# Kernel tuning notes

Hardware: AMD Instinct MI355X
Metric: run time of the kernel (lower is better)

## Reference

```python
import jax, jax.numpy as jnp
from jax import lax
import numpy as np

T, B, D, H = 4096, 32, 512, 256


def setup_inputs() -> dict:
    key = jax.random.key(0)
    ks = jax.random.split(key, 8)
    s_ih = 1.0 / np.sqrt(H)
    inp = {
        "x": jax.random.normal(ks[0], (T, B, D), dtype=jnp.float32),
        "reset": jax.random.randint(ks[1], (T, B), 0, 2, dtype=jnp.int32),
        # PyTorch nn.LSTM params, gate order (i, f, g, o)
        "W_ih": jax.random.uniform(ks[2], (4 * H, D), jnp.float32, -s_ih, s_ih),
        "W_hh": jax.random.uniform(ks[3], (4 * H, H), jnp.float32, -s_ih, s_ih),
        "b_ih": jax.random.uniform(ks[4], (4 * H,), jnp.float32, -s_ih, s_ih),
        "b_hh": jax.random.uniform(ks[5], (4 * H,), jnp.float32, -s_ih, s_ih),
        "W_proj": jax.random.uniform(ks[6], (1, H), jnp.float32, -s_ih, s_ih),
        "b_proj": jax.random.uniform(ks[7], (1,), jnp.float32, -s_ih, s_ih),
    }
    return inp


def _lstm_with_reset(x, reset, W_ih, W_hh, b_ih, b_hh):
    # Precompute input contribution for all timesteps: [T, B, 4H]
    xW = jnp.einsum("tbd,gd->tbg", x, W_ih) + b_ih + b_hh
    h0 = jnp.zeros((x.shape[1], H), x.dtype)
    c0 = jnp.zeros((x.shape[1], H), x.dtype)

    def step(carry, inp):
        h, c = carry
        xw, r = inp
        keep = (1 - r).astype(h.dtype)[:, None]  # zero state at episode starts
        h = h * keep
        c = c * keep
        gates = xw + h @ W_hh.T  # [B, 4H]
        i, f, g, o = jnp.split(gates, 4, axis=-1)
        c = jax.nn.sigmoid(f) * c + jax.nn.sigmoid(i) * jnp.tanh(g)
        h = jax.nn.sigmoid(o) * jnp.tanh(c)
        return (h, c), h

    (_, _), hs = lax.scan(step, (h0, c0), (xW, reset))
    return hs  # [T, B, H]


def reference(x, reset, W_ih, W_hh, b_ih, b_hh, W_proj, b_proj):
    hs = _lstm_with_reset(x, reset, W_ih, W_hh, b_ih, b_hh)
    return hs @ W_proj.T + b_proj  # [T, B, 1]
```

## Files before the change

### kernel.cpp

```cpp
#include <hip/hip_runtime.h>
#include <cstdint>
#include <cstddef>

#define T_DIM 4096
#define B_DIM 32
#define D_DIM 512
#define H_DIM 256
#define G_DIM 1024
#define HSTR 264

typedef _Float16 h8 __attribute__((ext_vector_type(8)));
typedef float f4 __attribute__((ext_vector_type(4)));

__global__ void seg_build_kernel(const int* __restrict__ reset,
                                 unsigned* __restrict__ starts,
                                 unsigned* __restrict__ segcnt) {
  __shared__ unsigned cnts[256];
  __shared__ unsigned offs[256];
  const int b = blockIdx.x;
  const int tid = threadIdx.x;
  const int t0 = tid * 16;
  unsigned c = 0;
  for (int e = 0; e < 16; ++e) {
    int t = t0 + e;
    bool pred = (t == 0) || (reset[t * B_DIM + b] != 0);
    c += pred ? 1u : 0u;
  }
  cnts[tid] = c;
  __syncthreads();
  if (tid == 0) {
    unsigned run = 0;
    for (int i = 0; i < 256; ++i) { unsigned v = cnts[i]; offs[i] = run; run += v; }
    segcnt[b] = run;
  }
  __syncthreads();
  unsigned o = (unsigned)b * 4096u + offs[tid];
  for (int e = 0; e < 16; ++e) {
    int t = t0 + e;
    bool pred = (t == 0) || (reset[t * B_DIM + b] != 0);
    if (pred) { starts[o++] = (unsigned)t; }
  }
}

__global__ void seg_flat_kernel(const unsigned* __restrict__ starts,
                                const unsigned* __restrict__ segcnt,
                                uint2* __restrict__ flat,
                                unsigned* __restrict__ meta) {
  __shared__ unsigned offs;
  const int b = blockIdx.x;
  const int tid = threadIdx.x;
  if (tid == 0) {
    unsigned o = 0;
    for (int i = 0; i < b; ++i) o += segcnt[i];
    offs = o;
    if (b == 31) meta[1] = o + segcnt[31];
    if (b == 0) meta[0] = 0u;
  }
  __syncthreads();
  const unsigned cnt = segcnt[b];
  const unsigned off = offs;
  for (unsigned s = tid; s < cnt; s += 256) {
    unsigned t0 = starts[b * 4096u + s];
    unsigned t1 = (s + 1 < cnt) ? starts[b * 4096u + s + 1] : 4096u;
    flat[off + s] = make_uint2(t0 | ((unsigned)b << 16), t1);
  }
}

__global__ void wpack_kernel(const float* __restrict__ Whh,
                             _Float16* __restrict__ wpack) {
  int gid = blockIdx.x * 256 + threadIdx.x;
  int nt = gid >> 9;
  int rem = gid & 511;
  int ks = rem >> 6;
  int l = rem & 63;
  int n = nt * 16 + (l & 15);
  int k = ks * 32 + (l >> 4) * 8;
  const float* src = Whh + (size_t)n * H_DIM + k;
  f4 v0 = *(const f4*)src;
  f4 v1 = *(const f4*)(src + 4);
  h8 wv = {(_Float16)v0.x, (_Float16)v0.y, (_Float16)v0.z, (_Float16)v0.w,
           (_Float16)v1.x, (_Float16)v1.y, (_Float16)v1.z, (_Float16)v1.w};
  *(h8*)(wpack + (size_t)gid * 8) = wv;
}

#define BM 128
#define BN 128
#define BK 32

__global__ __launch_bounds__(256) void xw_gemm_kernel(
    const float* __restrict__ X, const float* __restrict__ Wih,
    const float* __restrict__ bih, const float* __restrict__ bhh,
    _Float16* __restrict__ xw) {
  __shared__ _Float16 As[BM * BK];
  __shared__ _Float16 Bs[BN * BK];
  const int tid = threadIdx.x;
  const int lane = tid & 63;
  const int wave = tid >> 6;
  const size_t m0 = (size_t)blockIdx.y * BM;
  const int n0 = blockIdx.x * BN;
  const int wm = (wave & 1) * 64;
  const int wn = (wave >> 1) * 64;
  const int q = lane >> 4;
  const int r = lane & 15;

  f4 acc[4][4];
#pragma unroll
  for (int i = 0; i < 4; ++i)
#pragma unroll
    for (int j = 0; j < 4; ++j) { f4 z = {0.f, 0.f, 0.f, 0.f}; acc[i][j] = z; }

  const int srow = tid >> 1;
  const int kh = (tid & 1) * 16;

  for (int k0 = 0; k0 < D_DIM; k0 += BK) {
    const float* ax = X + (m0 + (size_t)srow) * D_DIM + k0 + kh;
    const float* bx = Wih + ((size_t)(n0 + srow)) * D_DIM + k0 + kh;
    f4 a0 = *(const f4*)(ax);
    f4 a1 = *(const f4*)(ax + 4);
    f4 a2 = *(const f4*)(ax + 8);
    f4 a3 = *(const f4*)(ax + 12);
    f4 b0 = *(const f4*)(bx);
    f4 b1 = *(const f4*)(bx + 4);
    f4 b2 = *(const f4*)(bx + 8);
    f4 b3 = *(const f4*)(bx + 12);
    h8 ha0 = {(_Float16)a0.x, (_Float16)a0.y, (_Float16)a0.z, (_Float16)a0.w,
              (_Float16)a1.x, (_Float16)a1.y, (_Float16)a1.z, (_Float16)a1.w};
    h8 ha1 = {(_Float16)a2.x, (_Float16)a2.y, (_Float16)a2.z, (_Float16)a2.w,
              (_Float16)a3.x, (_Float16)a3.y, (_Float16)a3.z, (_Float16)a3.w};
    h8 hb0 = {(_Float16)b0.x, (_Float16)b0.y, (_Float16)b0.z, (_Float16)b0.w,
              (_Float16)b1.x, (_Float16)b1.y, (_Float16)b1.z, (_Float16)b1.w};
    h8 hb1 = {(_Float16)b2.x, (_Float16)b2.y, (_Float16)b2.z, (_Float16)b2.w,
              (_Float16)b3.x, (_Float16)b3.y, (_Float16)b3.z, (_Float16)b3.w};
    *(h8*)(As + srow * BK + kh) = ha0;
    *(h8*)(As + srow * BK + kh + 8) = ha1;
    *(h8*)(Bs + srow * BK + kh) = hb0;
    *(h8*)(Bs + srow * BK + kh + 8) = hb1;
    __syncthreads();

    h8 af[4], bf[4];
#pragma unroll
    for (int mi = 0; mi < 4; ++mi)
      af[mi] = *(const h8*)(As + (wm + mi * 16 + r) * BK + q * 8);
#pragma unroll
    for (int ni = 0; ni < 4; ++ni)
      bf[ni] = *(const h8*)(Bs + (wn + ni * 16 + r) * BK + q * 8);
#pragma unroll
    for (int mi = 0; mi < 4; ++mi)
#pragma unroll
      for (int ni = 0; ni < 4; ++ni)
        acc[mi][ni] = __builtin_amdgcn_mfma_f32_16x16x32_f16(af[mi], bf[ni], acc[mi][ni], 0, 0, 0);
    __syncthreads();
  }

#pragma unroll
  for (int mi = 0; mi < 4; ++mi) {
#pragma unroll
    for (int ni = 0; ni < 4; ++ni) {
      int n = n0 + wn + ni * 16 + r;
      float bias = bih[n] + bhh[n];
#pragma unroll
      for (int reg = 0; reg < 4; ++reg) {
        size_t m = m0 + (size_t)(wm + mi * 16 + q * 4 + reg);
        xw[m * G_DIM + n] = (_Float16)(acc[mi][ni][reg] + bias);
      }
    }
  }
}

__device__ __forceinline__ float sigmf(float x) { return 1.f / (1.f + __expf(-x)); }
__device__ __forceinline__ float tanhf_(float x) {
  float e = __expf(-2.f * fabsf(x));
  float r = (1.f - e) / (1.f + e);
  return copysignf(r, x);
}
__device__ __forceinline__ f4 MF(h8 a, h8 b, f4 c) {
  return __builtin_amdgcn_mfma_f32_16x16x32_f16(a, b, c, 0, 0, 0);
}

#define WPK(g, ks) ((const h8*)(wpack + (((size_t)(((g)*16 + w) * 8 + (ks))) * 64 + l) * 8))
#define WLD(g, ks2) (*(const h8*)(Wlds + ((((ks2)*64) + ((g)*16 + w)) * 64 + l) * 8))
#define ARD(mt, ks) (*(const h8*)(Hbuf + (16*(mt) + r16) * HSTR + (ks)*32 + q*8))

#define MFMA8(B0, B1, B2, B3, KS)                          \
  a0 = ARD(0, KS); a1 = ARD(1, KS);                        \
  acc00 = MF(a0, B0, acc00); acc10 = MF(a1, B0, acc10);    \
  acc01 = MF(a0, B1, acc01); acc11 = MF(a1, B1, acc11);    \
  acc02 = MF(a0, B2, acc02); acc12 = MF(a1, B2, acc12);    \
  acc03 = MF(a0, B3, acc03); acc13 = MF(a1, B3, acc13);

#define XWADD(ACC, RB, G) {                                          \
  int nb = (G)*512 + nbase2;                                         \
  f4 xv;                                                             \
  xv.x = (float)*(const _Float16*)(xwc + RB.x + nb);                 \
  xv.y = (float)*(const _Float16*)(xwc + RB.y + nb);                 \
  xv.z = (float)*(const _Float16*)(xwc + RB.z + nb);                 \
  xv.w = (float)*(const _Float16*)(xwc + RB.w + nb);                 \
  ACC += xv; }

#define CONTROL_STEP do {                                                    \
  int m = tid;                                                               \
  if (alivef[m]) {                                                           \
    unsigned oi = outix[m];                                                  \
    if (oi != 0xFFFFFFFFu) {                                                 \
      float s = bp;                                                          \
      _Pragma("unroll") for (int ww = 0; ww < 16; ++ww) s += pbuf[ww][m];    \
      out[oi] = s;                                                           \
    }                                                                        \
    int t = tcur[m] + 1;                                                     \
    if (t < tend[m]) {                                                       \
      tcur[m] = t; keepm[m] = 1.f;                                           \
      unsigned row = (unsigned)t * 32u + (unsigned)bcol[m];                  \
      trowB[m] = row * 2048u; outix[m] = row;                                \
    } else {                                                                 \
      unsigned idx = atomicAdd(ctr, 1u);                                     \
      if (idx < nseg) {                                                      \
        uint2 sg = flat[idx];                                                \
        int t0s = (int)(sg.x & 0xFFFFu); int bb = (int)(sg.x >> 16);         \
        tcur[m] = t0s; tend[m] = (int)sg.y; bcol[m] = bb; keepm[m] = 0.f;    \
        unsigned row = (unsigned)t0s * 32u + (unsigned)bb;                   \
        trowB[m] = row * 2048u; outix[m] = row;                              \
        h8 zz = {0,0,0,0,0,0,0,0};                                           \
        _Pragma("unroll") for (int i2 = 0; i2 < 33; ++i2)                    \
          *(h8*)(Hbuf + (size_t)m * HSTR + i2 * 8) = zz;                     \
      } else {                                                               \
        alivef[m] = 0; outix[m] = 0xFFFFFFFFu; trowB[m] = 0;                 \
        keepm[m] = 0.f;                                                      \
      }                                                                      \
    }                                                                        \
  }                                                                          \
} while (0)

__global__ __launch_bounds__(1024, 4) void lstm_scan_mfma(
    const _Float16* __restrict__ xw,
    const _Float16* __restrict__ wpack,
    const float* __restrict__ Wproj,
    const float* __restrict__ bproj,
    const uint2* __restrict__ flat,
    unsigned* __restrict__ meta,
    float* __restrict__ out) {
  __shared__ __align__(16) _Float16 Wlds[2 * 64 * 64 * 8];
  __shared__ __align__(16) _Float16 Hbuf[32 * HSTR];
  __shared__ __align__(16) float pbuf[16][32];
  __shared__ __align__(16) unsigned trowB[32];
  __shared__ __align__(16) float keepm[32];
  __shared__ unsigned outix[32];
  __shared__ int tcur[32], tend[32], bcol[32], alivef[32];

  const int tid = threadIdx.x;
  const int l = tid & 63;
  const int w = tid >> 6;
  const int q = l >> 4;
  const int r16 = l & 15;
  const int hh = 16 * w + r16;
  const int nbase2 = hh * 2;
  const char* xwc = (const char*)xw;
  unsigned* ctr = meta;
  const unsigned nseg = meta[1];

  for (int it = 0; it < 8; ++it) {
    int idx = it * 1024 + tid;
    int ks2 = idx >> 12;
    int nt = (idx >> 6) & 63;
    int ll = idx & 63;
    *(h8*)(Wlds + (size_t)idx * 8) =
        *(const h8*)(wpack + (((size_t)(nt * 8 + ks2 + 1)) * 64 + ll) * 8);
  }
  for (int i = tid; i < 32 * HSTR / 8; i += 1024) {
    h8 z = {0,0,0,0,0,0,0,0};
    *(h8*)(Hbuf + (size_t)i * 8) = z;
  }
  h8 wb0 = *WPK(0, 0), wb1 = *WPK(1, 0), wb2 = *WPK(2, 0), wb3 = *WPK(3, 0);
  const float wpv = Wproj[hh];
  const float bp = bproj[0];
  if (tid < 32) {
    alivef[tid] = 1; tcur[tid] = 0; tend[tid] = 0; bcol[tid] = 0;
    outix[tid] = 0xFFFFFFFFu; trowB[tid] = 0; keepm[tid] = 0.f;
  }
  float cst[8] = {0, 0, 0, 0, 0, 0, 0, 0};
  float pr[8];
  __syncthreads();
  if (tid < 32) CONTROL_STEP;
  int nalive = __syncthreads_count(tid < 32 ? alivef[tid] : 0);

  while (nalive > 0) {
    f4 z4 = {0.f, 0.f, 0.f, 0.f};
    f4 acc00 = z4, acc01 = z4, acc02 = z4, acc03 = z4;
    f4 acc10 = z4, acc11 = z4, acc12 = z4, acc13 = z4;
    h8 a0, a1;
    h8 s0 = *WPK(0, 3), s1 = *WPK(1, 3), s2 = *WPK(2, 3), s3 = *WPK(3, 3);
    MFMA8(wb0, wb1, wb2, wb3, 0)
    h8 u0 = *WPK(0, 4), u1 = *WPK(1, 4), u2 = *WPK(2, 4), u3 = *WPK(3, 4);
    { h8 b0 = WLD(0, 0), b1 = WLD(1, 0), b2 = WLD(2, 0), b3 = WLD(3, 0);
      MFMA8(b0, b1, b2, b3, 1) }
    { h8 b0 = WLD(0, 1), b1 = WLD(1, 1), b2 = WLD(2, 1), b3 = WLD(3, 1);
      MFMA8(b0, b1, b2, b3, 2) }
    MFMA8(s0, s1, s2, s3, 3)
    s0 = *WPK(0, 5); s1 = *WPK(1, 5); s2 = *WPK(2, 5); s3 = *WPK(3, 5);
    MFMA8(u0, u1, u2, u3, 4)
    u0 = *WPK(0, 6); u1 = *WPK(1, 6); u2 = *WPK(2, 6); u3 = *WPK(3, 6);
    MFMA8(s0, s1, s2, s3, 5)
    s0 = *WPK(0, 7); s1 = *WPK(1, 7); s2 = *WPK(2, 7); s3 = *WPK(3, 7);
    MFMA8(u0, u1, u2, u3, 6)
    MFMA8(s0, s1, s2, s3, 7)

    __syncthreads();

    uint4 rb0 = *(const uint4*)&trowB[q * 4];
    uint4 rb1 = *(const uint4*)&trowB[16 + q * 4];
    XWADD(acc00, rb0, 0) XWADD(acc01, rb0, 1) XWADD(acc02, rb0, 2) XWADD(acc03, rb0, 3)
    XWADD(acc10, rb1, 0) XWADD(acc11, rb1, 1) XWADD(acc12, rb1, 2) XWADD(acc13, rb1, 3)

    f4 kp0 = *(const f4*)&keepm[q * 4];
    f4 kp1 = *(const f4*)&keepm[16 + q * 4];
#pragma unroll
    for (int r = 0; r < 4; ++r) {
      float gi = sigmf(acc00[r]);
      float gf = sigmf(acc01[r]);
      float gg = tanhf_(acc02[r]);
      float go = sigmf(acc03[r]);
      float cn = gf * (cst[r] * kp0[r]) + gi * gg;
      cst[r] = cn;
      float hv = go * tanhf_(cn);
      Hbuf[(q * 4 + r) * HSTR + hh] = (_Float16)hv;
      pr[r] = hv * wpv;
    }
#pragma unroll
    for (int r = 0; r < 4; ++r) {
      float gi = sigmf(acc10[r]);
      float gf = sigmf(acc11[r]);
      float gg = tanhf_(acc12[r]);
      float go = sigmf(acc13[r]);
      float cn = gf * (cst[4 + r] * kp1[r]) + gi * gg;
      cst[4 + r] = cn;
      float hv = go * tanhf_(cn);
      Hbuf[(16 + q * 4 + r) * HSTR + hh] = (_Float16)hv;
      pr[4 + r] = hv * wpv;
    }
#pragma unroll
    for (int j = 0; j < 8; ++j) {
      pr[j] += __shfl_xor(pr[j], 1);
      pr[j] += __shfl_xor(pr[j], 2);
      pr[j] += __shfl_xor(pr[j], 4);
      pr[j] += __shfl_xor(pr[j], 8);
    }
    if (r16 == 0) {
#pragma unroll
      for (int j = 0; j < 8; ++j)
        pbuf[w][16 * (j >> 2) + q * 4 + (j & 3)] = pr[j];
    }

    __syncthreads();
    if (tid < 32) CONTROL_STEP;
    nalive = __syncthreads_count(tid < 32 ? alivef[tid] : 0);
  }
}

extern "C" void kernel_launch(void* const* d_in, const int* in_sizes, int n_in,
                              void* d_out, int out_size, void* d_ws, size_t ws_size,
                              hipStream_t stream) {
  const float* x = (const float*)d_in[0];
  const int* reset = (const int*)d_in[1];
  const float* Wih = (const float*)d_in[2];
  const float* Whh = (const float*)d_in[3];
  const float* bih = (const float*)d_in[4];
  const float* bhh = (const float*)d_in[5];
  const float* Wproj = (const float*)d_in[6];
  const float* bproj = (const float*)d_in[7];
  float* out = (float*)d_out;

  char* ws = (char*)d_ws;
  _Float16* xw = (_Float16*)ws;
  unsigned* starts = (unsigned*)(ws + 268435456ULL);
  unsigned* segcnt = (unsigned*)(ws + 268959744ULL);
  uint2* flat = (uint2*)(ws + 268959872ULL);
  _Float16* wpack = (_Float16*)(ws + 270008448ULL);
  unsigned* meta = (unsigned*)(ws + 270532736ULL);

  hipLaunchKernelGGL(seg_build_kernel, dim3(32), dim3(256), 0, stream,
                     reset, starts, segcnt);
  hipLaunchKernelGGL(seg_flat_kernel, dim3(32), dim3(256), 0, stream,
                     starts, segcnt, flat, meta);
  hipLaunchKernelGGL(wpack_kernel, dim3(128), dim3(256), 0, stream,
                     Whh, wpack);
  hipLaunchKernelGGL(xw_gemm_kernel, dim3(8, 1024), dim3(256), 0, stream,
                     x, Wih, bih, bhh, xw);
  hipLaunchKernelGGL(lstm_scan_mfma, dim3(256), dim3(1024), 0, stream,
                     xw, wpack, Wproj, bproj, flat, meta, out);
}
```

Measured before the change: 1.446 ms.

## Sort segments by length, halve scan block size, remap GEMM tiles per XCD

Adds a counting sort that orders reset-delimited segments longest-first, so the dynamic work queue in the scan kernel schedules long segments early and trims tail imbalance. The scan kernel drops from 1024 to 512 threads; each wave now handles twice as many hidden columns and keeps 4 of the 8 K-slices of W_hh in registers. The remaining slices are split between two streamed from global memory and two held in LDS. The xW GEMM grid is flattened and remapped so neighbouring tiles land on the same XCD for better L2 reuse, and sigmoid/tanh switch to a fast reciprocal form. These changes raise register pressure and add a serial single-block sort kernel, and the new tanh form may lose accuracy for large inputs.

```diff
diff --git a/kernel.cpp b/kernel.cpp
--- a/kernel.cpp
+++ b/kernel.cpp
@@ -8,17 +8,20 @@
 #define H_DIM 256
 #define G_DIM 1024
 #define HSTR 264
+#define NBUCK 128
 
 typedef _Float16 h8 __attribute__((ext_vector_type(8)));
 typedef float f4 __attribute__((ext_vector_type(4)));
 
 __global__ void seg_build_kernel(const int* __restrict__ reset,
                                  unsigned* __restrict__ starts,
-                                 unsigned* __restrict__ segcnt) {
+                                 unsigned* __restrict__ segcnt,
+                                 unsigned* __restrict__ hist) {
   __shared__ unsigned cnts[256];
   __shared__ unsigned offs[256];
   const int b = blockIdx.x;
   const int tid = threadIdx.x;
+  if (b == 0 && tid < NBUCK) hist[tid] = 0u;
   const int t0 = tid * 16;
   unsigned c = 0;
   for (int e = 0; e < 16; ++e) {
@@ -44,7 +47,8 @@
 
 __global__ void seg_flat_kernel(const unsigned* __restrict__ starts,
                                 const unsigned* __restrict__ segcnt,
-                                uint2* __restrict__ flat,
+                                uint2* __restrict__ flat2,
+                                unsigned* __restrict__ hist,
                                 unsigned* __restrict__ meta) {
   __shared__ unsigned offs;
   const int b = blockIdx.x;
@@ -62,7 +66,30 @@
   for (unsigned s = tid; s < cnt; s += 256) {
     unsigned t0 = starts[b * 4096u + s];
     unsigned t1 = (s + 1 < cnt) ? starts[b * 4096u + s + 1] : 4096u;
-    flat[off + s] = make_uint2(t0 | ((unsigned)b << 16), t1);
+    flat2[off + s] = make_uint2(t0 | ((unsigned)b << 16), t1);
+    unsigned len = t1 - t0;
+    atomicAdd(&hist[min(len, (unsigned)NBUCK) - 1u], 1u);
+  }
+}
+
+__global__ void seg_sort_kernel(const uint2* __restrict__ flat2,
+                                const unsigned* __restrict__ hist,
+                                uint2* __restrict__ flat,
+                                const unsigned* __restrict__ meta) {
+  __shared__ unsigned cur[NBUCK];
+  const unsigned nseg = meta[1];
+  const int tid = threadIdx.x;
+  if (tid == 0) {
+    unsigned run = 0;
+    for (int k = NBUCK - 1; k >= 0; --k) { cur[k] = run; run += hist[k]; }
+  }
+  __syncthreads();
+  for (unsigned i = tid; i < nseg; i += 1024) {
+    uint2 e = flat2[i];
+    unsigned len = e.y - (e.x & 0xFFFFu);
+    unsigned bk = min(len, (unsigned)NBUCK) - 1u;
+    unsigned pos = atomicAdd(&cur[bk], 1u);
+    flat[pos] = e;
   }
 }
 
@@ -96,8 +123,11 @@
   const int tid = threadIdx.x;
   const int lane = tid & 63;
   const int wave = tid >> 6;
-  const size_t m0 = (size_t)blockIdx.y * BM;
-  const int n0 = blockIdx.x * BN;
+  const unsigned wg = blockIdx.x;
+  const unsigned xcd = wg & 7u;
+  const unsigned idx = wg >> 3;
+  const size_t m0 = (size_t)(xcd * 128u + (idx >> 3)) * BM;
+  const int n0 = (int)(idx & 7u) * BN;
   const int wm = (wave & 1) * 64;
   const int wn = (wave >> 1) * 64;
   const int q = lane >> 4;
@@ -167,35 +197,60 @@
   }
 }
 
-__device__ __forceinline__ float sigmf(float x) { return 1.f / (1.f + __expf(-x)); }
+__device__ __forceinline__ float sigmf(float x) {
+  return __builtin_amdgcn_rcpf(1.f + __expf(-x));
+}
 __device__ __forceinline__ float tanhf_(float x) {
-  float e = __expf(-2.f * fabsf(x));
-  float r = (1.f - e) / (1.f + e);
-  return copysignf(r, x);
+  return 2.f * __builtin_amdgcn_rcpf(1.f + __expf(-2.f * x)) - 1.f;
 }
 __device__ __forceinline__ f4 MF(h8 a, h8 b, f4 c) {
   return __builtin_amdgcn_mfma_f32_16x16x32_f16(a, b, c, 0, 0, 0);
 }
 
-#define WPK(g, ks) ((const h8*)(wpack + (((size_t)(((g)*16 + w) * 8 + (ks))) * 64 + l) * 8))
-#define WLD(g, ks2) (*(const h8*)(Wlds + ((((ks2)*64) + ((g)*16 + w)) * 64 + l) * 8))
+#define WPKp(g, j, ks) \
+  ((const h8*)(wpack + (((size_t)((((g)*16 + 2*w + (j)) * 8 + (ks))) * 64 + l) * 8)))
+#define WLDp(g, j, ks2) \
+  (*(const h8*)(Wlds + ((((ks2)*64) + ((g)*16 + 2*w + (j))) * 64 + l) * 8))
 #define ARD(mt, ks) (*(const h8*)(Hbuf + (16*(mt) + r16) * HSTR + (ks)*32 + q*8))
 
-#define MFMA8(B0, B1, B2, B3, KS)                          \
-  a0 = ARD(0, KS); a1 = ARD(1, KS);                        \
-  acc00 = MF(a0, B0, acc00); acc10 = MF(a1, B0, acc10);    \
-  acc01 = MF(a0, B1, acc01); acc11 = MF(a1, B1, acc11);    \
-  acc02 = MF(a0, B2, acc02); acc12 = MF(a1, B2, acc12);    \
-  acc03 = MF(a0, B3, acc03); acc13 = MF(a1, B3, acc13);
-
-#define XWADD(ACC, RB, G) {                                          \
-  int nb = (G)*512 + nbase2;                                         \
-  f4 xv;                                                             \
-  xv.x = (float)*(const _Float16*)(xwc + RB.x + nb);                 \
-  xv.y = (float)*(const _Float16*)(xwc + RB.y + nb);                 \
-  xv.z = (float)*(const _Float16*)(xwc + RB.z + nb);                 \
-  xv.w = (float)*(const _Float16*)(xwc + RB.w + nb);                 \
-  ACC += xv; }
+#define MFK_REG(KS) do {                                                   \
+  h8 a0_ = ARD(0, KS), a1_ = ARD(1, KS);                                   \
+  _Pragma("unroll") for (int g = 0; g < 4; ++g)                            \
+  _Pragma("unroll") for (int j = 0; j < 2; ++j) {                          \
+    acc[0][g][j] = MF(a0_, wr[g][j][KS], acc[0][g][j]);                    \
+    acc[1][g][j] = MF(a1_, wr[g][j][KS], acc[1][g][j]); }                  \
+} while (0)
+
+#define MFK_LDS(KS2, KS) do {                                              \
+  h8 a0_ = ARD(0, KS), a1_ = ARD(1, KS);                                   \
+  _Pragma("unroll") for (int g = 0; g < 4; ++g)                            \
+  _Pragma("unroll") for (int j = 0; j < 2; ++j) {                          \
+    h8 b_ = WLDp(g, j, KS2);                                               \
+    acc[0][g][j] = MF(a0_, b_, acc[0][g][j]);                              \
+    acc[1][g][j] = MF(a1_, b_, acc[1][g][j]); }                            \
+} while (0)
+
+#define MFK_STR(KS) do {                                                   \
+  h8 a0_ = ARD(0, KS), a1_ = ARD(1, KS);                                   \
+  _Pragma("unroll") for (int g = 0; g < 4; ++g)                            \
+  _Pragma("unroll") for (int j = 0; j < 2; ++j) {                          \
+    acc[0][g][j] = MF(a0_, sreg[g][j], acc[0][g][j]);                      \
+    acc[1][g][j] = MF(a1_, sreg[g][j], acc[1][g][j]); }                    \
+} while (0)
+
+#define LOAD_STR(KS) do {                                                  \
+  _Pragma("unroll") for (int g = 0; g < 4; ++g)                            \
+  _Pragma("unroll") for (int j = 0; j < 2; ++j)                            \
+    sreg[g][j] = *WPKp(g, j, KS);                                          \
+} while (0)
+
+#define XWG(MT, G, J, RB, NB) do {                                         \
+  f4 xv;                                                                   \
+  xv.x = (float)*(const _Float16*)(xwc + RB.x + (G)*512 + (NB));           \
+  xv.y = (float)*(const _Float16*)(xwc + RB.y + (G)*512 + (NB));           \
+  xv.z = (float)*(const _Float16*)(xwc + RB.z + (G)*512 + (NB));           \
+  xv.w = (float)*(const _Float16*)(xwc + RB.w + (G)*512 + (NB));           \
+  acc[MT][G][J] += xv; } while (0)
 
 #define CONTROL_STEP do {                                                    \
   int m = tid;                                                               \
@@ -203,7 +258,7 @@
     unsigned oi = outix[m];                                                  \
     if (oi != 0xFFFFFFFFu) {                                                 \
       float s = bp;                                                          \
-      _Pragma("unroll") for (int ww = 0; ww < 16; ++ww) s += pbuf[ww][m];    \
+      _Pragma("unroll") for (int ww = 0; ww < 8; ++ww) s += pbuf[ww][m];     \
       out[oi] = s;                                                           \
     }                                                                        \
     int t = tcur[m] + 1;                                                     \
@@ -230,7 +285,7 @@
   }                                                                          \
 } while (0)
 
-__global__ __launch_bounds__(1024, 4) void lstm_scan_mfma(
+__global__ __launch_bounds__(512, 2) void lstm_scan_mfma(
     const _Float16* __restrict__ xw,
     const _Float16* __restrict__ wpack,
     const float* __restrict__ Wproj,
@@ -240,7 +295,7 @@
     float* __restrict__ out) {
   __shared__ __align__(16) _Float16 Wlds[2 * 64 * 64 * 8];
   __shared__ __align__(16) _Float16 Hbuf[32 * HSTR];
-  __shared__ __align__(16) float pbuf[16][32];
+  __shared__ __align__(16) float pbuf[8][32];
   __shared__ __align__(16) unsigned trowB[32];
   __shared__ __align__(16) float keepm[32];
   __shared__ unsigned outix[32];
@@ -251,102 +306,146 @@
   const int w = tid >> 6;
   const int q = l >> 4;
   const int r16 = l & 15;
-  const int hh = 16 * w + r16;
-  const int nbase2 = hh * 2;
   const char* xwc = (const char*)xw;
   unsigned* ctr = meta;
   const unsigned nseg = meta[1];
 
-  for (int it = 0; it < 8; ++it) {
-    int idx = it * 1024 + tid;
+  for (int it = 0; it < 16; ++it) {
+    int idx = it * 512 + tid;
     int ks2 = idx >> 12;
     int nt = (idx >> 6) & 63;
     int ll = idx & 63;
     *(h8*)(Wlds + (size_t)idx * 8) =
-        *(const h8*)(wpack + (((size_t)(nt * 8 + ks2 + 1)) * 64 + ll) * 8);
-  }
-  for (int i = tid; i < 32 * HSTR / 8; i += 1024) {
+        *(const h8*)(wpack + (((size_t)(nt * 8 + ks2 + 4)) * 64 + ll) * 8);
+  }
+  for (int i = tid; i < 32 * HSTR / 8; i += 512) {
     h8 z = {0,0,0,0,0,0,0,0};
     *(h8*)(Hbuf + (size_t)i * 8) = z;
   }
-  h8 wb0 = *WPK(0, 0), wb1 = *WPK(1, 0), wb2 = *WPK(2, 0), wb3 = *WPK(3, 0);
-  const float wpv = Wproj[hh];
+  h8 wr[4][2][4];
+#pragma unroll
+  for (int g = 0; g < 4; ++g)
+#pragma unroll
+    for (int j = 0; j < 2; ++j)
+#pragma unroll
+      for (int ks = 0; ks < 4; ++ks)
+        wr[g][j][ks] = *WPKp(g, j, ks);
+
+  const float wpv0 = Wproj[32 * w + r16];
+  const float wpv1 = Wproj[32 * w + 16 + r16];
   const float bp = bproj[0];
   if (tid < 32) {
     alivef[tid] = 1; tcur[tid] = 0; tend[tid] = 0; bcol[tid] = 0;
     outix[tid] = 0xFFFFFFFFu; trowB[tid] = 0; keepm[tid] = 0.f;
   }
-  float cst[8] = {0, 0, 0, 0, 0, 0, 0, 0};
-  float pr[8];
+  float cst[16];
+#pragma unroll
+  for (int i = 0; i < 16; ++i) cst[i] = 0.f;
   __syncthreads();
   if (tid < 32) CONTROL_STEP;
   int nalive = __syncthreads_count(tid < 32 ? alivef[tid] : 0);
 
   while (nalive > 0) {
     f4 z4 = {0.f, 0.f, 0.f, 0.f};
-    f4 acc00 = z4, acc01 = z4, acc02 = z4, acc03 = z4;
-    f4 acc10 = z4, acc11 = z4, acc12 = z4, acc13 = z4;
-    h8 a0, a1;
-    h8 s0 = *WPK(0, 3), s1 = *WPK(1, 3), s2 = *WPK(2, 3), s3 = *WPK(3, 3);
-    MFMA8(wb0, wb1, wb2, wb3, 0)
-    h8 u0 = *WPK(0, 4), u1 = *WPK(1, 4), u2 = *WPK(2, 4), u3 = *WPK(3, 4);
-    { h8 b0 = WLD(0, 0), b1 = WLD(1, 0), b2 = WLD(2, 0), b3 = WLD(3, 0);
-      MFMA8(b0, b1, b2, b3, 1) }
-    { h8 b0 = WLD(0, 1), b1 = WLD(1, 1), b2 = WLD(2, 1), b3 = WLD(3, 1);
-      MFMA8(b0, b1, b2, b3, 2) }
-    MFMA8(s0, s1, s2, s3, 3)
-    s0 = *WPK(0, 5); s1 = *WPK(1, 5); s2 = *WPK(2, 5); s3 = *WPK(3, 5);
-    MFMA8(u0, u1, u2, u3, 4)
-    u0 = *WPK(0, 6); u1 = *WPK(1, 6); u2 = *WPK(2, 6); u3 = *WPK(3, 6);
-    MFMA8(s0, s1, s2, s3, 5)
-    s0 = *WPK(0, 7); s1 = *WPK(1, 7); s2 = *WPK(2, 7); s3 = *WPK(3, 7);
-    MFMA8(u0, u1, u2, u3, 6)
-    MFMA8(s0, s1, s2, s3, 7)
+    f4 acc[2][4][2];
+#pragma unroll
+    for (int mt = 0; mt < 2; ++mt)
+#pragma unroll
+      for (int g = 0; g < 4; ++g)
+#pragma unroll
+        for (int j = 0; j < 2; ++j) acc[mt][g][j] = z4;
+    h8 sreg[4][2];
+
+    LOAD_STR(6);
+    MFK_REG(0);
+    MFK_STR(6);
+    LOAD_STR(7);
+    MFK_REG(1);
+    MFK_STR(7);
+    MFK_REG(2);
+    MFK_REG(3);
+    MFK_LDS(0, 4);
+    MFK_LDS(1, 5);
 
     __syncthreads();
 
     uint4 rb0 = *(const uint4*)&trowB[q * 4];
     uint4 rb1 = *(const uint4*)&trowB[16 + q * 4];
-    XWADD(acc00, rb0, 0) XWADD(acc01, rb0, 1) XWADD(acc02, rb0, 2) XWADD(acc03, rb0, 3)
-    XWADD(acc10, rb1, 0) XWADD(acc11, rb1, 1) XWADD(acc12, rb1, 2) XWADD(acc13, rb1, 3)
+    const int nb0 = w * 64 + r16 * 2;
+    const int nb1 = nb0 + 32;
+    XWG(0, 0, 0, rb0, nb0); XWG(0, 0, 1, rb0, nb1);
+    XWG(0, 1, 0, rb0, nb0); XWG(0, 1, 1, rb0, nb1);
+    XWG(0, 2, 0, rb0, nb0); XWG(0, 2, 1, rb0, nb1);
+    XWG(0, 3, 0, rb0, nb0); XWG(0, 3, 1, rb0, nb1);
+    XWG(1, 0, 0, rb1, nb0); XWG(1, 0, 1, rb1, nb1);
+    XWG(1, 1, 0, rb1, nb0); XWG(1, 1, 1, rb1, nb1);
+    XWG(1, 2, 0, rb1, nb0); XWG(1, 2, 1, rb1, nb1);
+    XWG(1, 3, 0, rb1, nb0); XWG(1, 3, 1, rb1, nb1);
 
     f4 kp0 = *(const f4*)&keepm[q * 4];
     f4 kp1 = *(const f4*)&keepm[16 + q * 4];
+    float pr[8];
 #pragma unroll
     for (int r = 0; r < 4; ++r) {
-      float gi = sigmf(acc00[r]);
-      float gf = sigmf(acc01[r]);
-      float gg = tanhf_(acc02[r]);
-      float go = sigmf(acc03[r]);
-      float cn = gf * (cst[r] * kp0[r]) + gi * gg;
-      cst[r] = cn;
-      float hv = go * tanhf_(cn);
-      Hbuf[(q * 4 + r) * HSTR + hh] = (_Float16)hv;
-      pr[r] = hv * wpv;
+      {
+        float gi = sigmf(acc[0][0][0][r]);
+        float gf = sigmf(acc[0][1][0][r]);
+        float gg = tanhf_(acc[0][2][0][r]);
+        float go = sigmf(acc[0][3][0][r]);
+        float cn = gf * (cst[r] * kp0[r]) + gi * gg;
+        cst[r] = cn;
+        float hv = go * tanhf_(cn);
+        Hbuf[(q * 4 + r) * HSTR + 32 * w + r16] = (_Float16)hv;
+        pr[r] = hv * wpv0;
+      }
+      {
+        float gi = sigmf(acc[0][0][1][r]);
+        float gf = sigmf(acc[0][1][1][r]);
+        float gg = tanhf_(acc[0][2][1][r]);
+        float go = sigmf(acc[0][3][1][r]);
+        float cn = gf * (cst[4 + r] * kp0[r]) + gi * gg;
+        cst[4 + r] = cn;
+        float hv = go * tanhf_(cn);
+        Hbuf[(q * 4 + r) * HSTR + 32 * w + 16 + r16] = (_Float16)hv;
+        pr[r] += hv * wpv1;
+      }
     }
 #pragma unroll
     for (int r = 0; r < 4; ++r) {
-      float gi = sigmf(acc10[r]);
-      float gf = sigmf(acc11[r]);
-      float gg = tanhf_(acc12[r]);
-      float go = sigmf(acc13[r]);
-      float cn = gf * (cst[4 + r] * kp1[r]) + gi * gg;
-      cst[4 + r] = cn;
-      float hv = go * tanhf_(cn);
-      Hbuf[(16 + q * 4 + r) * HSTR + hh] = (_Float16)hv;
-      pr[4 + r] = hv * wpv;
+      {
+        float gi = sigmf(acc[1][0][0][r]);
+        float gf = sigmf(acc[1][1][0][r]);
+        float gg = tanhf_(acc[1][2][0][r]);
+        float go = sigmf(acc[1][3][0][r]);
+        float cn = gf * (cst[8 + r] * kp1[r]) + gi * gg;
+        cst[8 + r] = cn;
+        float hv = go * tanhf_(cn);
+        Hbuf[(16 + q * 4 + r) * HSTR + 32 * w + r16] = (_Float16)hv;
+        pr[4 + r] = hv * wpv0;
+      }
+      {
+        float gi = sigmf(acc[1][0][1][r]);
+        float gf = sigmf(acc[1][1][1][r]);
+        float gg = tanhf_(acc[1][2][1][r]);
+        float go = sigmf(acc[1][3][1][r]);
+        float cn = gf * (cst[12 + r] * kp1[r]) + gi * gg;
+        cst[12 + r] = cn;
+        float hv = go * tanhf_(cn);
+        Hbuf[(16 + q * 4 + r) * HSTR + 32 * w + 16 + r16] = (_Float16)hv;
+        pr[4 + r] += hv * wpv1;
+      }
     }
 #pragma unroll
-    for (int j = 0; j < 8; ++j) {
-      pr[j] += __shfl_xor(pr[j], 1);
-      pr[j] += __shfl_xor(pr[j], 2);
-      pr[j] += __shfl_xor(pr[j], 4);
-      pr[j] += __shfl_xor(pr[j], 8);
+    for (int jj = 0; jj < 8; ++jj) {
+      pr[jj] += __shfl_xor(pr[jj], 1);
+      pr[jj] += __shfl_xor(pr[jj], 2);
+      pr[jj] += __shfl_xor(pr[jj], 4);
+      pr[jj] += __shfl_xor(pr[jj], 8);
     }
     if (r16 == 0) {
 #pragma unroll
-      for (int j = 0; j < 8; ++j)
-        pbuf[w][16 * (j >> 2) + q * 4 + (j & 3)] = pr[j];
+      for (int jj = 0; jj < 8; ++jj)
+        pbuf[w][16 * (jj >> 2) + q * 4 + (jj & 3)] = pr[jj];
     }
 
     __syncthreads();
@@ -375,15 +474,19 @@
   uint2* flat = (uint2*)(ws + 268959872ULL);
   _Float16* wpack = (_Float16*)(ws + 270008448ULL);
   unsigned* meta = (unsigned*)(ws + 270532736ULL);
+  uint2* flat2 = (uint2*)ws;
+  unsigned* hist = (unsigned*)(ws + 1048576ULL);
 
   hipLaunchKernelGGL(seg_build_kernel, dim3(32), dim3(256), 0, stream,
-                     reset, starts, segcnt);
+                     reset, starts, segcnt, hist);
   hipLaunchKernelGGL(seg_flat_kernel, dim3(32), dim3(256), 0, stream,
-                     starts, segcnt, flat, meta);
+                     starts, segcnt, flat2, hist, meta);
+  hipLaunchKernelGGL(seg_sort_kernel, dim3(1), dim3(1024), 0, stream,
+                     flat2, hist, flat, meta);
   hipLaunchKernelGGL(wpack_kernel, dim3(128), dim3(256), 0, stream,
                      Whh, wpack);
-  hipLaunchKernelGGL(xw_gemm_kernel, dim3(8, 1024), dim3(256), 0, stream,
+  hipLaunchKernelGGL(xw_gemm_kernel, dim3(8192), dim3(256), 0, stream,
                      x, Wih, bih, bhh, xw);
-  hipLaunchKernelGGL(lstm_scan_mfma, dim3(256), dim3(1024), 0, stream,
+  hipLaunchKernelGGL(lstm_scan_mfma, dim3(256), dim3(512), 0, stream,
                      xw, wpack, Wproj, bproj, flat, meta, out);
 }
```

Result: slower. 1.499 ms (+3.7%).
